# Kernel optimization log

Hardware: AMD Instinct MI355X
Metric: run time of the kernel (lower is better)

## Reference

```python
import jax, jax.numpy as jnp
import numpy as np

N_EMBD = 1024
N_HEAD = 16
HEAD_SIZE = N_EMBD // N_HEAD  # 64
BLOCK_SIZE = 2048
HIDDEN = 2 * N_EMBD  # SwiGLU hidden
LN_EPS = 1e-5


def layernorm(x, w, b):
    m = jnp.mean(x, axis=-1, keepdims=True)
    v = jnp.mean(jnp.square(x - m), axis=-1, keepdims=True)
    return (x - m) * jax.lax.rsqrt(v + LN_EPS) * w + b


def rotate_half(x):
    # interleaved halves, exactly as the torch code: stack((-x2, x1)).reshape
    x1 = x[..., 0::2]
    x2 = x[..., 1::2]
    return jnp.stack((-x2, x1), axis=-1).reshape(x.shape)


def rope_tables(T, hd):
    inv_freq = 1.0 / (10000.0 ** (jnp.arange(0, hd, 2, dtype=jnp.float32) / hd))
    t = jnp.arange(T, dtype=jnp.float32)
    freqs = t[:, None] * inv_freq[None, :]           # [T, hd/2]
    emb = jnp.concatenate([freqs, freqs], axis=-1)   # [T, hd]
    return jnp.cos(emb), jnp.sin(emb)


def setup_inputs() -> dict:
    key = jax.random.key(0)
    ks = jax.random.split(key, 12)
    s = 0.02
    d = {
        "x": jax.random.normal(ks[0], (2, BLOCK_SIZE, N_EMBD), dtype=jnp.float32),
        "ln1_w": jnp.ones((N_EMBD,), jnp.float32),
        "ln1_b": jnp.zeros((N_EMBD,), jnp.float32),
        "ln2_w": jnp.ones((N_EMBD,), jnp.float32),
        "ln2_b": jnp.zeros((N_EMBD,), jnp.float32),
        # per-head projections, stored (H, C, hd); equivalent to x @ W.T in torch
        "Wq": jax.random.normal(ks[1], (N_HEAD, N_EMBD, HEAD_SIZE), jnp.float32) * s,
        "Wk": jax.random.normal(ks[2], (N_HEAD, N_EMBD, HEAD_SIZE), jnp.float32) * s,
        "Wv": jax.random.normal(ks[3], (N_HEAD, N_EMBD, HEAD_SIZE), jnp.float32) * s,
        "proj_w": jax.random.normal(ks[4], (N_EMBD, N_EMBD), jnp.float32) * s,
        "proj_b": jnp.zeros((N_EMBD,), jnp.float32),
        # SwiGLU MLP
        "w_w": jax.random.normal(ks[5], (N_EMBD, HIDDEN), jnp.float32) * s,
        "w_b": jnp.zeros((HIDDEN,), jnp.float32),
        "v_w": jax.random.normal(ks[6], (N_EMBD, HIDDEN), jnp.float32) * s,
        "v_b": jnp.zeros((HIDDEN,), jnp.float32),
        "p_w": jax.random.normal(ks[7], (HIDDEN, N_EMBD), jnp.float32) * s,
        "p_b": jnp.zeros((N_EMBD,), jnp.float32),
    }
    return d


def reference(x, ln1_w, ln1_b, ln2_w, ln2_b, Wq, Wk, Wv, proj_w, proj_b,
              w_w, w_b, v_w, v_b, p_w, p_b):
    B, T, C = x.shape
    # --- attention sub-block ---
    h = layernorm(x, ln1_w, ln1_b)
    q = jnp.einsum('btc,hcd->bhtd', h, Wq)
    k = jnp.einsum('btc,hcd->bhtd', h, Wk)
    v = jnp.einsum('btc,hcd->bhtd', h, Wv)
    cos, sin = rope_tables(T, HEAD_SIZE)  # [T, hd]
    cos = cos[None, None]
    sin = sin[None, None]
    q = q * cos + rotate_half(q) * sin
    k = k * cos + rotate_half(k) * sin
    scale = 1.0 / jnp.sqrt(jnp.float32(HEAD_SIZE))
    scores = jnp.einsum('bhtd,bhsd->bhts', q, k) * scale  # [B,H,T,T]
    causal = jnp.tril(jnp.ones((T, T), dtype=bool))
    scores = jnp.where(causal[None, None], scores, -jnp.inf)
    att = jax.nn.softmax(scores, axis=-1)
    o = jnp.einsum('bhts,bhsd->bhtd', att, v)
    o = o.transpose(0, 2, 1, 3).reshape(B, T, C)  # concat heads
    sa = o @ proj_w + proj_b
    x = x + sa
    # --- SwiGLU FFN sub-block ---
    h2 = layernorm(x, ln2_w, ln2_b)
    a = h2 @ w_w + w_b
    a = a * jax.nn.sigmoid(a)  # swish
    b = h2 @ v_w + v_b
    ff = (a * b) @ p_w + p_b
    return x + ff
```

## Files before the change

kernel.cpp:

```cpp
#include <hip/hip_runtime.h>
#include <math.h>

#define N_EMBD    1024
#define N_HEAD    16
#define HEAD_SIZE 64
#define T_SEQ     2048
#define BATCH     2
#define HIDDEN    2048
#define ROWS      4096

typedef __attribute__((ext_vector_type(8))) short bf16x8;
typedef __attribute__((ext_vector_type(4))) float f32x4;
typedef __attribute__((ext_vector_type(16))) float f32x16;
typedef unsigned short u16;

__device__ __forceinline__ u16 f2bf(float x) {
    union { float f; unsigned u; } v; v.f = x;
    unsigned r = v.u + 0x7fffu + ((v.u >> 16) & 1u);
    return (u16)(r >> 16);
}
__device__ __forceinline__ float bf2f(u16 h) {
    union { unsigned u; float f; } v; v.u = ((unsigned)h) << 16;
    return v.f;
}
__device__ __forceinline__ unsigned cvtpk_bf16(float lo, float hi) {
    unsigned r;
    asm volatile("v_cvt_pk_bf16_f32 %0, %1, %2" : "=v"(r) : "v"(lo), "v"(hi));
    return r;
}
__device__ __forceinline__ void gload16(const void* g, void* lds) {
    __builtin_amdgcn_global_load_lds((const __attribute__((address_space(1))) void*)g,
                                     (__attribute__((address_space(3))) void*)lds, 16, 0, 0);
}

__device__ __forceinline__ void wtrans_body(const float* s, u16* d, int ldS, int ldD,
                                            int k0, int n0, float Ts[64][65])
{
    const int tid = threadIdx.x;
    const int rr = tid >> 4, c4 = (tid & 15) * 4;
#pragma unroll
    for (int i = 0; i < 4; i++) {
        float4 v = *(const float4*)(s + (size_t)(k0 + rr + i * 16) * ldS + n0 + c4);
        Ts[rr + i * 16][c4 + 0] = v.x;
        Ts[rr + i * 16][c4 + 1] = v.y;
        Ts[rr + i * 16][c4 + 2] = v.z;
        Ts[rr + i * 16][c4 + 3] = v.w;
    }
    __syncthreads();
    const int nr = tid >> 2, kc = (tid & 3) * 16;
#pragma unroll
    for (int j = 0; j < 4; j++) {
        u16 t0 = f2bf(Ts[kc + j * 4 + 0][nr]);
        u16 t1 = f2bf(Ts[kc + j * 4 + 1][nr]);
        u16 t2 = f2bf(Ts[kc + j * 4 + 2][nr]);
        u16 t3 = f2bf(Ts[kc + j * 4 + 3][nr]);
        *(ushort4*)(d + (size_t)(n0 + nr) * ldD + k0 + kc + j * 4) = make_ushort4(t0, t1, t2, t3);
    }
}

__global__ __launch_bounds__(256) void wtrans(const float* __restrict__ src, u16* __restrict__ dst,
                                              int ldS, int ldD)
{
    __shared__ float Ts[64][65];
    wtrans_body(src, dst, ldS, ldD, blockIdx.x * 64, blockIdx.y * 64, Ts);
}

__global__ __launch_bounds__(256) void wtrans_qkv(const float* __restrict__ Wq, const float* __restrict__ Wk,
                                                  const float* __restrict__ Wv, u16* __restrict__ dst)
{
    __shared__ float Ts[64][65];
    const int z = blockIdx.z;
    const int which = z >> 4;
    const float* s = (which == 0 ? Wq : (which == 1 ? Wk : Wv)) + (size_t)(z & 15) * 65536;
    wtrans_body(s, dst + (size_t)z * 65536, HEAD_SIZE, N_EMBD, blockIdx.x * 64, 0, Ts);
}

__global__ __launch_bounds__(256) void wtrans_wv(const float* __restrict__ ww, const float* __restrict__ vv,
                                                 u16* __restrict__ dw, u16* __restrict__ dv)
{
    __shared__ float Ts[64][65];
    const int z = blockIdx.z;
    const float* s = (z >> 5) ? vv : ww;
    u16* d = (z >> 5) ? dv : dw;
    wtrans_body(s, d, HIDDEN, N_EMBD, blockIdx.x * 64, (z & 31) * 64, Ts);
}

__global__ __launch_bounds__(256) void ln_kernel(const float* __restrict__ x,
                                                 const float* __restrict__ w,
                                                 const float* __restrict__ b,
                                                 u16* __restrict__ out)
{
    const int row = blockIdx.x;
    const int tid = threadIdx.x;
    const float* xr = x + (size_t)row * N_EMBD;
    float4 v = *(const float4*)(xr + tid * 4);
    float s  = v.x + v.y + v.z + v.w;
    float s2 = v.x*v.x + v.y*v.y + v.z*v.z + v.w*v.w;
#pragma unroll
    for (int off = 32; off; off >>= 1) {
        s  += __shfl_xor(s, off);
        s2 += __shfl_xor(s2, off);
    }
    __shared__ float ss[4], ss2[4];
    if ((tid & 63) == 0) { ss[tid >> 6] = s; ss2[tid >> 6] = s2; }
    __syncthreads();
    s  = ss[0] + ss[1] + ss[2] + ss[3];
    s2 = ss2[0] + ss2[1] + ss2[2] + ss2[3];
    const float mean = s * (1.0f / N_EMBD);
    const float var  = s2 * (1.0f / N_EMBD) - mean * mean;
    const float rstd = rsqrtf(var + 1e-5f);
    float4 wv = *(const float4*)(w + tid * 4);
    float4 bv = *(const float4*)(b + tid * 4);
    ushort4 st = make_ushort4(f2bf((v.x - mean) * rstd * wv.x + bv.x),
                              f2bf((v.y - mean) * rstd * wv.y + bv.y),
                              f2bf((v.z - mean) * rstd * wv.z + bv.z),
                              f2bf((v.w - mean) * rstd * wv.w + bv.w));
    *(ushort4*)(out + (size_t)row * N_EMBD + tid * 4) = st;
}

__global__ __launch_bounds__(256) void rope_kernel(u16* __restrict__ q, u16* __restrict__ k)
{
    const int u = blockIdx.x * 256 + threadIdx.x;
    const int i  = u & 31;
    const int t  = (u >> 5) & (T_SEQ - 1);
    const int bh = u >> 16;
    const size_t base = ((size_t)bh * T_SEQ + t) * HEAD_SIZE + 2 * i;
    const float L = 0.28782313662425572f;
    const int i0 = (2 * i) & 31, i1 = (2 * i + 1) & 31;
    float c0, s0, c1, s1;
    sincosf((float)t * __expf(-(float)i0 * L), &s0, &c0);
    sincosf((float)t * __expf(-(float)i1 * L), &s1, &c1);
    float a0 = bf2f(q[base]), a1 = bf2f(q[base + 1]);
    q[base]     = f2bf(a0 * c0 - a1 * s0);
    q[base + 1] = f2bf(a1 * c1 + a0 * s1);
    float b0 = bf2f(k[base]), b1 = bf2f(k[base + 1]);
    k[base]     = f2bf(b0 * c0 - b1 * s0);
    k[base + 1] = f2bf(b1 * c1 + b0 * s1);
}


__global__ __launch_bounds__(256) void gemm_br(const u16* __restrict__ A, const u16* __restrict__ Bt,
                                               const float* __restrict__ bias, const float* __restrict__ resid,
                                               float* __restrict__ Cf,
                                               int N, int K)
{
    __shared__ __align__(16) u16 As[2][128 * 64];
    __shared__ __align__(16) u16 Bs[2][64 * 64];
    const int tid = threadIdx.x, w = tid >> 6, l = tid & 63, l15 = l & 15, l4 = l >> 4;
    const int wm = w >> 1, wn = w & 1;
    const int n0 = blockIdx.x * 64, m0 = blockIdx.y * 128;
    f32x4 acc[4][2] = {};
    const int NT = K >> 6;

    auto stage = [&](int buf, int k0) {
#pragma unroll
        for (int c = 0; c < 4; c++) {
            const int slot = c * 256 + tid;
            const int row = slot >> 3;
            const int sw = ((slot & 7) * 16) ^ ((row & 7) << 4);
            gload16((const char*)(A + (size_t)(m0 + row) * K + k0) + sw, (char*)&As[buf][0] + slot * 16);
        }
#pragma unroll
        for (int c = 0; c < 2; c++) {
            const int slot = c * 256 + tid;
            const int row = slot >> 3;
            const int sw = ((slot & 7) * 16) ^ ((row & 7) << 4);
            gload16((const char*)(Bt + (size_t)(n0 + row) * K + k0) + sw, (char*)&Bs[buf][0] + slot * 16);
        }
    };

    stage(0, 0);
    __syncthreads();
    int cur = 0;
    for (int t = 0; t < NT; t++) {
        if (t + 1 < NT) stage(cur ^ 1, (t + 1) << 6);
#pragma unroll
        for (int ks = 0; ks < 2; ks++) {
            const int cb = ks * 64 + l4 * 16;
            bf16x8 af[4], bf[2];
#pragma unroll
            for (int mt = 0; mt < 4; mt++) {
                const int row = wm * 64 + mt * 16 + l15;
                af[mt] = *(const bf16x8*)((const char*)&As[cur][0] + row * 128 + (cb ^ ((row & 7) << 4)));
            }
#pragma unroll
            for (int u = 0; u < 2; u++) {
                const int row = wn * 32 + u * 16 + l15;
                bf[u] = *(const bf16x8*)((const char*)&Bs[cur][0] + row * 128 + (cb ^ ((row & 7) << 4)));
            }
#pragma unroll
            for (int mt = 0; mt < 4; mt++)
#pragma unroll
                for (int u = 0; u < 2; u++)
                    acc[mt][u] = __builtin_amdgcn_mfma_f32_16x16x32_bf16(af[mt], bf[u], acc[mt][u], 0, 0, 0);
        }
        __syncthreads();
        cur ^= 1;
    }
#pragma unroll
    for (int mt = 0; mt < 4; mt++) {
#pragma unroll
        for (int u = 0; u < 2; u++) {
            const int n = n0 + wn * 32 + u * 16 + l15;
            const float bi = bias[n];
#pragma unroll
            for (int r = 0; r < 4; r++) {
                const int m = m0 + wm * 64 + mt * 16 + l4 * 4 + r;
                const size_t idx = (size_t)m * N + n;
                Cf[idx] = acc[mt][u][r] + bi + resid[idx];
            }
        }
    }
}

__global__ __launch_bounds__(256, 4) void gemm_qkv(const u16* __restrict__ A, const u16* __restrict__ Bt,
                                                   u16* __restrict__ qo, u16* __restrict__ ko, u16* __restrict__ vto)
{
    __shared__ __align__(16) u16 As[2][64 * 64];
    __shared__ __align__(16) u16 Bs[2][64 * 64];
    const int tid = threadIdx.x, w = tid >> 6, l = tid & 63, l15 = l & 15, l4 = l >> 4;
    const int wm = w >> 1, wn = w & 1;
    const int n0 = blockIdx.x * 128, m0 = blockIdx.y * 128;
    const int K = N_EMBD;
    f32x4 acc[4][4] = {};
    const int NT = K >> 5;

    auto stage = [&](int buf, int k0) {
#pragma unroll
        for (int c = 0; c < 2; c++) {
            const int slot = c * 256 + tid;
            const int r2 = slot >> 3;
            const int w16u = (slot & 7) ^ (r2 & 7);
            const int grow = (w16u >> 2) * 64 + r2;
            const int kc = w16u & 3;
            gload16(A  + (size_t)(m0 + grow) * K + k0 + kc * 8, (char*)&As[buf][0] + slot * 16);
            gload16(Bt + (size_t)(n0 + grow) * K + k0 + kc * 8, (char*)&Bs[buf][0] + slot * 16);
        }
    };

    stage(0, 0);
    __syncthreads();
    int cur = 0;
    for (int t = 0; t < NT; t++) {
        if (t + 1 < NT) stage(cur ^ 1, (t + 1) << 5);
        bf16x8 af[4], bf[4];
#pragma unroll
        for (int q4 = 0; q4 < 4; q4++) {
            const int ga = wm * 64 + q4 * 16 + l15;
            const int ra = ga & 63, ha = ga >> 6;
            af[q4] = *(const bf16x8*)((const char*)&As[cur][0] + ra * 128 + (((ha << 2) | l4) ^ (ra & 7)) * 16);
            const int gb = wn * 64 + q4 * 16 + l15;
            const int rb = gb & 63, hb = gb >> 6;
            bf[q4] = *(const bf16x8*)((const char*)&Bs[cur][0] + rb * 128 + (((hb << 2) | l4) ^ (rb & 7)) * 16);
        }
#pragma unroll
        for (int mt = 0; mt < 4; mt++)
#pragma unroll
            for (int nt = 0; nt < 4; nt++)
                acc[mt][nt] = __builtin_amdgcn_mfma_f32_16x16x32_bf16(af[mt], bf[nt], acc[mt][nt], 0, 0, 0);
        __syncthreads();
        cur ^= 1;
    }
#pragma unroll
    for (int mt = 0; mt < 4; mt++) {
#pragma unroll
        for (int nt = 0; nt < 4; nt++) {
            const int n = n0 + wn * 64 + nt * 16 + l15;
            const int which = n >> 10, hd = (n >> 6) & 15, dd = n & 63;
            const int mb = m0 + wm * 64 + mt * 16 + l4 * 4;
            const int bI = mb >> 11, tq = mb & (T_SEQ - 1);
            if (which == 2) {
                ushort4 st = make_ushort4(f2bf(acc[mt][nt][0]), f2bf(acc[mt][nt][1]),
                                          f2bf(acc[mt][nt][2]), f2bf(acc[mt][nt][3]));
                *(ushort4*)(vto + ((size_t)(bI * N_HEAD + hd) * HEAD_SIZE + dd) * T_SEQ + tq) = st;
            } else {
                u16* dst = (which == 0) ? qo : ko;
#pragma unroll
                for (int r = 0; r < 4; r++)
                    dst[((size_t)(bI * N_HEAD + hd) * T_SEQ + tq + r) * HEAD_SIZE + dd] = f2bf(acc[mt][nt][r]);
            }
        }
    }
}

__global__ __launch_bounds__(256, 4) void gemm_glu(const u16* __restrict__ A, const u16* __restrict__ Bw,
                                                   const u16* __restrict__ Bv,
                                                   const float* __restrict__ wb, const float* __restrict__ vb,
                                                   u16* __restrict__ G)
{
    __shared__ __align__(16) u16 As[2][64 * 64];
    __shared__ __align__(16) u16 Bws[2][32 * 64];
    __shared__ __align__(16) u16 Bvs[2][32 * 64];
    const int tid = threadIdx.x, w = tid >> 6, l = tid & 63, l15 = l & 15, l4 = l >> 4;
    const int wm = w >> 1, wn = w & 1;
    const int n0 = blockIdx.x * 64, m0 = blockIdx.y * 128;
    const int K = N_EMBD;
    f32x4 accA[4][2] = {};
    f32x4 accB[4][2] = {};
    const int NT = K >> 5;

    auto stage = [&](int buf, int k0) {
#pragma unroll
        for (int c = 0; c < 2; c++) {
            const int slot = c * 256 + tid;
            const int r2 = slot >> 3;
            const int w16u = (slot & 7) ^ (r2 & 7);
            const int grow = (w16u >> 2) * 64 + r2;
            const int kc = w16u & 3;
            gload16(A + (size_t)(m0 + grow) * K + k0 + kc * 8, (char*)&As[buf][0] + slot * 16);
        }
        {
            const int slot = tid;
            const int r2 = slot >> 3;
            const int w16u = (slot & 7) ^ (r2 & 7);
            const int grow = (w16u >> 2) * 32 + r2;
            const int kc = w16u & 3;
            gload16(Bw + (size_t)(n0 + grow) * K + k0 + kc * 8, (char*)&Bws[buf][0] + slot * 16);
            gload16(Bv + (size_t)(n0 + grow) * K + k0 + kc * 8, (char*)&Bvs[buf][0] + slot * 16);
        }
    };

    stage(0, 0);
    __syncthreads();
    int cur = 0;
    for (int t = 0; t < NT; t++) {
        if (t + 1 < NT) stage(cur ^ 1, (t + 1) << 5);
        bf16x8 af[4], bwf[2], bvf[2];
#pragma unroll
        for (int q4 = 0; q4 < 4; q4++) {
            const int ga = wm * 64 + q4 * 16 + l15;
            const int ra = ga & 63, ha = ga >> 6;
            af[q4] = *(const bf16x8*)((const char*)&As[cur][0] + ra * 128 + (((ha << 2) | l4) ^ (ra & 7)) * 16);
        }
#pragma unroll
        for (int u = 0; u < 2; u++) {
            const int gb = wn * 32 + u * 16 + l15;
            const int rb = gb & 31, hb = gb >> 5;
            const int off = rb * 128 + (((hb << 2) | l4) ^ (rb & 7)) * 16;
            bwf[u] = *(const bf16x8*)((const char*)&Bws[cur][0] + off);
            bvf[u] = *(const bf16x8*)((const char*)&Bvs[cur][0] + off);
        }
#pragma unroll
        for (int mt = 0; mt < 4; mt++)
#pragma unroll
            for (int u = 0; u < 2; u++) {
                accA[mt][u] = __builtin_amdgcn_mfma_f32_16x16x32_bf16(af[mt], bwf[u], accA[mt][u], 0, 0, 0);
                accB[mt][u] = __builtin_amdgcn_mfma_f32_16x16x32_bf16(af[mt], bvf[u], accB[mt][u], 0, 0, 0);
            }
        __syncthreads();
        cur ^= 1;
    }
#pragma unroll
    for (int mt = 0; mt < 4; mt++) {
#pragma unroll
        for (int u = 0; u < 2; u++) {
            const int n = n0 + wn * 32 + u * 16 + l15;
            const float wbi = wb[n], vbi = vb[n];
#pragma unroll
            for (int r = 0; r < 4; r++) {
                const int m = m0 + wm * 64 + mt * 16 + l4 * 4 + r;
                const float a  = accA[mt][u][r] + wbi;
                const float bb = accB[mt][u][r] + vbi;
                G[(size_t)m * HIDDEN + n] = f2bf(a / (1.f + __expf(-a)) * bb);
            }
        }
    }
}

__global__ __launch_bounds__(256, 2) void attn_mfma(const u16* __restrict__ q, const u16* __restrict__ k,
                                                    const u16* __restrict__ vt, u16* __restrict__ o)
{
    __shared__ __align__(16) u16 Kb[2][128 * 64];
    __shared__ __align__(16) u16 Vb[2][64 * 128];
    __shared__ float ml[2][32];
    const int tid = threadIdx.x, l = tid & 63, l31 = l & 31, hh2 = (l >> 5) & 1;
    const int wid  = tid >> 6;
    const int qsub = wid >> 1;
    const int par  = wid & 1;
    const int bh  = blockIdx.x;
    const int qtb = (int)gridDim.y - 1 - (int)blockIdx.y;
    const int qt  = qtb * 2 + qsub;
    const int qw0 = qt * 32;
    const int nc  = qtb + 1;
    const int npairs = (nc + 1) >> 1;
    const u16* qb  = q  + (size_t)bh * T_SEQ * HEAD_SIZE;
    const u16* kbg = k  + (size_t)bh * T_SEQ * HEAD_SIZE;
    const u16* vbg = vt + (size_t)bh * HEAD_SIZE * T_SEQ;

    bf16x8 qf[4];
    {
        const u16* qr = qb + (size_t)(qw0 + l31) * HEAD_SIZE + hh2 * 8;
#pragma unroll
        for (int kk = 0; kk < 4; kk++) qf[kk] = *(const bf16x8*)(qr + kk * 16);
    }

    f32x16 oacc0 = {}, oacc1 = {};
    float lrow = 0.f;
    const float qs = 0.125f * 1.44269504088896f;
    const float M0 = 20.f;

    auto stage = [&](int buf, int s0p) {
#pragma unroll
        for (int c = 0; c < 4; c++) {
            const int slot = c * 256 + tid;
            const int row = slot >> 3, colb = (slot & 7) * 16;
            const int sw = colb ^ ((row & 7) << 4);
            gload16((const char*)(kbg + (size_t)(s0p + row) * HEAD_SIZE) + sw, (char*)&Kb[buf][0] + slot * 16);
        }
#pragma unroll
        for (int c = 0; c < 4; c++) {
            const int slot = c * 256 + tid;
            const int row = slot >> 4, col16 = slot & 15;
            const int sw = (col16 ^ (row & 15)) << 4;
            gload16((const char*)(vbg + (size_t)row * T_SEQ + s0p) + sw, (char*)&Vb[buf][0] + slot * 16);
        }
    };

    stage(0, 0);
    __syncthreads();
    int cur = 0;

    for (int j = 0; j < npairs; j++) {
        if (j + 1 < npairs) stage(cur ^ 1, (j + 1) * 128);

        const int cc = 2 * j + par;
        if (cc < nc) {
            const bool diag = (cc == nc - 1);
            const bool half = diag && !(qt & 1);

            f32x16 sa0 = {}, sa1 = {};
#pragma unroll
            for (int kk = 0; kk < 4; kk++) {
                const int row = par * 64 + l31;
                const int swz = (row & 7) << 4;
                const bf16x8 kf = *(const bf16x8*)((const char*)&Kb[cur][0] + row * 128 + ((kk * 32 + hh2 * 16) ^ swz));
                sa0 = __builtin_amdgcn_mfma_f32_32x32x16_bf16(kf, qf[kk], sa0, 0, 0, 0);
            }
            if (!half) {
#pragma unroll
                for (int kk = 0; kk < 4; kk++) {
                    const int row = par * 64 + 32 + l31;
                    const int swz = (row & 7) << 4;
                    const bf16x8 kf = *(const bf16x8*)((const char*)&Kb[cur][0] + row * 128 + ((kk * 32 + hh2 * 16) ^ swz));
                    sa1 = __builtin_amdgcn_mfma_f32_32x32x16_bf16(kf, qf[kk], sa1, 0, 0, 0);
                }
            }

            if (diag) {
#pragma unroll
                for (int reg = 0; reg < 16; reg++) {
                    const int R = (reg & 3) + 8 * (reg >> 2) + 4 * hh2;
                    if (R > l31) { if (qt & 1) sa1[reg] = -1e30f; else sa0[reg] = -1e30f; }
                }
            }

            float ls = 0.f;
#pragma unroll
            for (int reg = 0; reg < 16; reg++) {
                const float pv = exp2f(fmaf(sa0[reg], qs, -M0));
                sa0[reg] = pv;
                ls += pv;
            }
            if (!half) {
#pragma unroll
                for (int reg = 0; reg < 16; reg++) {
                    const float pv = exp2f(fmaf(sa1[reg], qs, -M0));
                    sa1[reg] = pv;
                    ls += pv;
                }
            }
            ls += __shfl_xor(ls, 32);
            lrow += ls;

            unsigned pkA[8], pkB[8];
#pragma unroll
            for (int jj = 0; jj < 8; jj++) pkA[jj] = cvtpk_bf16(sa0[2 * jj], sa0[2 * jj + 1]);
            if (!half) {
#pragma unroll
                for (int jj = 0; jj < 8; jj++) pkB[jj] = cvtpk_bf16(sa1[2 * jj], sa1[2 * jj + 1]);
            }

#pragma unroll
            for (int st = 0; st < 4; st++) {
                if (half && st >= 2) continue;
                const unsigned* pk = (st < 2) ? pkA : pkB;
                const int b = (st & 1) * 4;
                union { unsigned u[4]; bf16x8 v; } r;
                const unsigned s0w = (unsigned)__shfl_xor((int)pk[b + 0], 32);
                const unsigned s1w = (unsigned)__shfl_xor((int)pk[b + 1], 32);
                const unsigned s2w = (unsigned)__shfl_xor((int)pk[b + 2], 32);
                const unsigned s3w = (unsigned)__shfl_xor((int)pk[b + 3], 32);
                r.u[0] = hh2 ? s2w : pk[b + 0];
                r.u[1] = hh2 ? s3w : pk[b + 1];
                r.u[2] = hh2 ? pk[b + 2] : s0w;
                r.u[3] = hh2 ? pk[b + 3] : s1w;
#pragma unroll
                for (int dt = 0; dt < 2; dt++) {
                    const int row = dt * 32 + l31;
                    const int col16 = (par * 8 + st * 2 + hh2) ^ (row & 15);
                    const bf16x8 vf = *(const bf16x8*)((const char*)&Vb[cur][0] + row * 256 + col16 * 16);
                    if (dt == 0) oacc0 = __builtin_amdgcn_mfma_f32_32x32x16_bf16(vf, r.v, oacc0, 0, 0, 0);
                    else         oacc1 = __builtin_amdgcn_mfma_f32_32x32x16_bf16(vf, r.v, oacc1, 0, 0, 0);
                }
            }
        }
        __syncthreads();
        cur ^= 1;
    }

    float* obuf = (float*)&Kb[0][0] + (size_t)qsub * 2048;
    if (par == 1) {
#pragma unroll
        for (int reg = 0; reg < 16; reg++) {
            const int R = (reg & 3) + 8 * (reg >> 2) + 4 * hh2;
            obuf[R * 32 + l31] = oacc0[reg];
            obuf[(32 + R) * 32 + l31] = oacc1[reg];
        }
        if (hh2 == 0) ml[qsub][l31] = lrow;
    }
    __syncthreads();
    if (par == 0) {
        const float inv = 1.f / (lrow + ml[qsub][l31]);
        const int bI = bh >> 4, hd = bh & 15;
        u16* ob = o + ((size_t)(bI * T_SEQ + qw0 + l31)) * N_EMBD + hd * HEAD_SIZE;
#pragma unroll
        for (int g = 0; g < 4; g++) {
            const int d0a = g * 8 + hh2 * 4;
            float v0[4], v1[4];
#pragma unroll
            for (int r = 0; r < 4; r++) {
                const int R = d0a + r;
                v0[r] = (oacc0[4 * g + r] + obuf[R * 32 + l31]) * inv;
                v1[r] = (oacc1[4 * g + r] + obuf[(32 + R) * 32 + l31]) * inv;
            }
            *(ushort4*)(ob + d0a)      = make_ushort4(f2bf(v0[0]), f2bf(v0[1]), f2bf(v0[2]), f2bf(v0[3]));
            *(ushort4*)(ob + 32 + d0a) = make_ushort4(f2bf(v1[0]), f2bf(v1[1]), f2bf(v1[2]), f2bf(v1[3]));
        }
    }
}

extern "C" void kernel_launch(void* const* d_in, const int* in_sizes, int n_in,
                              void* d_out, int out_size, void* d_ws, size_t ws_size,
                              hipStream_t stream)
{
    (void)in_sizes; (void)n_in; (void)out_size; (void)ws_size;
    const float* x      = (const float*)d_in[0];
    const float* ln1_w  = (const float*)d_in[1];
    const float* ln1_b  = (const float*)d_in[2];
    const float* ln2_w  = (const float*)d_in[3];
    const float* ln2_b  = (const float*)d_in[4];
    const float* Wq     = (const float*)d_in[5];
    const float* Wk     = (const float*)d_in[6];
    const float* Wv     = (const float*)d_in[7];
    const float* proj_w = (const float*)d_in[8];
    const float* proj_b = (const float*)d_in[9];
    const float* w_w    = (const float*)d_in[10];
    const float* w_b    = (const float*)d_in[11];
    const float* v_w    = (const float*)d_in[12];
    const float* v_b    = (const float*)d_in[13];
    const float* p_w    = (const float*)d_in[14];
    const float* p_b    = (const float*)d_in[15];
    float* out = (float*)d_out;

    char* W = (char*)d_ws;
    u16*   Wqkv = (u16*)(W + 0);
    u16*   pwT  = (u16*)(W + 6291456);
    u16*   wwT  = (u16*)(W + 8388608);
    u16*   vvT  = (u16*)(W + 12582912);
    u16*   ppT  = (u16*)(W + 16777216);
    u16*   h    = (u16*)(W + 20971520);
    u16*   qB   = (u16*)(W + 29360128);
    u16*   kB   = (u16*)(W + 37748736);
    u16*   vtB  = (u16*)(W + 46137344);
    u16*   oB   = (u16*)(W + 54525952);
    float* x1   = (float*)(W + 62914560);
    u16*   ga   = qB;

    wtrans_qkv<<<dim3(16, 1, 48), 256, 0, stream>>>(Wq, Wk, Wv, Wqkv);
    wtrans_wv<<<dim3(16, 1, 64), 256, 0, stream>>>(w_w, v_w, wwT, vvT);
    wtrans<<<dim3(16, 16), 256, 0, stream>>>(proj_w, pwT, 1024, 1024);
    wtrans<<<dim3(32, 16), 256, 0, stream>>>(p_w, ppT, 1024, 2048);

    ln_kernel<<<ROWS, 256, 0, stream>>>(x, ln1_w, ln1_b, h);
    gemm_qkv<<<dim3(24, 32), 256, 0, stream>>>(h, Wqkv, qB, kB, vtB);
    rope_kernel<<<(BATCH * N_HEAD * T_SEQ * 32) / 256, 256, 0, stream>>>(qB, kB);
    attn_mfma<<<dim3(BATCH * N_HEAD, T_SEQ / 64), 256, 0, stream>>>(qB, kB, vtB, oB);
    gemm_br<<<dim3(16, 32), 256, 0, stream>>>(oB, pwT, proj_b, x, x1, N_EMBD, N_EMBD);
    ln_kernel<<<ROWS, 256, 0, stream>>>(x1, ln2_w, ln2_b, h);
    gemm_glu<<<dim3(32, 32), 256, 0, stream>>>(h, wwT, vvT, w_b, v_b, ga);
    gemm_br<<<dim3(16, 32), 256, 0, stream>>>(ga, ppT, p_b, x1, out, N_EMBD, HIDDEN);
}
```

Baseline: 212.7 us.

## Fuse RoPE into QKV GEMM epilogue and shrink attention KV tiles

Removes the standalone RoPE kernel and applies the rotation in the QKV GEMM epilogue, using a lane shuffle to fetch the paired element, so q/k are no longer re-read and re-written. Separately, the attention kernel now stages 64-key tiles instead of 128-key pairs, which halves its shared memory and raises the occupancy hint to 4 blocks, with each wave handling one 32-key half per iteration. The trade-offs are extra sincos work in the GEMM epilogue and more loop iterations and barriers in attention.

```diff
diff --git a/kernel.cpp b/kernel.cpp
--- a/kernel.cpp
+++ b/kernel.cpp
@@ -118,27 +118,6 @@
     *(ushort4*)(out + (size_t)row * N_EMBD + tid * 4) = st;
 }
 
-__global__ __launch_bounds__(256) void rope_kernel(u16* __restrict__ q, u16* __restrict__ k)
-{
-    const int u = blockIdx.x * 256 + threadIdx.x;
-    const int i  = u & 31;
-    const int t  = (u >> 5) & (T_SEQ - 1);
-    const int bh = u >> 16;
-    const size_t base = ((size_t)bh * T_SEQ + t) * HEAD_SIZE + 2 * i;
-    const float L = 0.28782313662425572f;
-    const int i0 = (2 * i) & 31, i1 = (2 * i + 1) & 31;
-    float c0, s0, c1, s1;
-    sincosf((float)t * __expf(-(float)i0 * L), &s0, &c0);
-    sincosf((float)t * __expf(-(float)i1 * L), &s1, &c1);
-    float a0 = bf2f(q[base]), a1 = bf2f(q[base + 1]);
-    q[base]     = f2bf(a0 * c0 - a1 * s0);
-    q[base + 1] = f2bf(a1 * c1 + a0 * s1);
-    float b0 = bf2f(k[base]), b1 = bf2f(k[base + 1]);
-    k[base]     = f2bf(b0 * c0 - b1 * s0);
-    k[base + 1] = f2bf(b1 * c1 + b0 * s1);
-}
-
-
 __global__ __launch_bounds__(256) void gemm_br(const u16* __restrict__ A, const u16* __restrict__ Bt,
                                                const float* __restrict__ bias, const float* __restrict__ resid,
                                                float* __restrict__ Cf,
@@ -261,6 +240,7 @@
         __syncthreads();
         cur ^= 1;
     }
+    const float Lr = 0.28782313662425572f;
 #pragma unroll
     for (int mt = 0; mt < 4; mt++) {
 #pragma unroll
@@ -275,9 +255,16 @@
                 *(ushort4*)(vto + ((size_t)(bI * N_HEAD + hd) * HEAD_SIZE + dd) * T_SEQ + tq) = st;
             } else {
                 u16* dst = (which == 0) ? qo : ko;
-#pragma unroll
-                for (int r = 0; r < 4; r++)
-                    dst[((size_t)(bI * N_HEAD + hd) * T_SEQ + tq + r) * HEAD_SIZE + dd] = f2bf(acc[mt][nt][r]);
+                const float fr = __expf(-(float)(dd & 31) * Lr);
+#pragma unroll
+                for (int r = 0; r < 4; r++) {
+                    const float v = acc[mt][nt][r];
+                    const float part = __shfl_xor(v, 1);
+                    float sn, cs;
+                    sincosf((float)(tq + r) * fr, &sn, &cs);
+                    const float ov = (dd & 1) ? fmaf(v, cs, part * sn) : fmaf(v, cs, -part * sn);
+                    dst[((size_t)(bI * N_HEAD + hd) * T_SEQ + tq + r) * HEAD_SIZE + dd] = f2bf(ov);
+                }
             }
         }
     }
@@ -367,11 +354,11 @@
     }
 }
 
-__global__ __launch_bounds__(256, 2) void attn_mfma(const u16* __restrict__ q, const u16* __restrict__ k,
+__global__ __launch_bounds__(256, 4) void attn_mfma(const u16* __restrict__ q, const u16* __restrict__ k,
                                                     const u16* __restrict__ vt, u16* __restrict__ o)
 {
-    __shared__ __align__(16) u16 Kb[2][128 * 64];
-    __shared__ __align__(16) u16 Vb[2][64 * 128];
+    __shared__ __align__(16) u16 Kb[2][64 * 64];
+    __shared__ __align__(16) u16 Vb[2][64 * 64];
     __shared__ float ml[2][32];
     const int tid = threadIdx.x, l = tid & 63, l31 = l & 31, hh2 = (l >> 5) & 1;
     const int wid  = tid >> 6;
@@ -382,7 +369,6 @@
     const int qt  = qtb * 2 + qsub;
     const int qw0 = qt * 32;
     const int nc  = qtb + 1;
-    const int npairs = (nc + 1) >> 1;
     const u16* qb  = q  + (size_t)bh * T_SEQ * HEAD_SIZE;
     const u16* kbg = k  + (size_t)bh * T_SEQ * HEAD_SIZE;
     const u16* vbg = vt + (size_t)bh * HEAD_SIZE * T_SEQ;
@@ -399,20 +385,20 @@
     const float qs = 0.125f * 1.44269504088896f;
     const float M0 = 20.f;
 
-    auto stage = [&](int buf, int s0p) {
-#pragma unroll
-        for (int c = 0; c < 4; c++) {
+    auto stage = [&](int buf, int s0) {
+#pragma unroll
+        for (int c = 0; c < 2; c++) {
             const int slot = c * 256 + tid;
-            const int row = slot >> 3, colb = (slot & 7) * 16;
-            const int sw = colb ^ ((row & 7) << 4);
-            gload16((const char*)(kbg + (size_t)(s0p + row) * HEAD_SIZE) + sw, (char*)&Kb[buf][0] + slot * 16);
-        }
-#pragma unroll
-        for (int c = 0; c < 4; c++) {
+            const int row = slot >> 3;
+            const int sw = ((slot & 7) * 16) ^ ((row & 7) << 4);
+            gload16((const char*)(kbg + (size_t)(s0 + row) * HEAD_SIZE) + sw, (char*)&Kb[buf][0] + slot * 16);
+        }
+#pragma unroll
+        for (int c = 0; c < 2; c++) {
             const int slot = c * 256 + tid;
-            const int row = slot >> 4, col16 = slot & 15;
-            const int sw = (col16 ^ (row & 15)) << 4;
-            gload16((const char*)(vbg + (size_t)row * T_SEQ + s0p) + sw, (char*)&Vb[buf][0] + slot * 16);
+            const int row = slot >> 3;
+            const int sw = ((slot & 7) * 16) ^ ((row & 7) << 4);
+            gload16((const char*)(vbg + (size_t)row * T_SEQ + s0) + sw, (char*)&Vb[buf][0] + slot * 16);
         }
     };
 
@@ -420,71 +406,43 @@
     __syncthreads();
     int cur = 0;
 
-    for (int j = 0; j < npairs; j++) {
-        if (j + 1 < npairs) stage(cur ^ 1, (j + 1) * 128);
-
-        const int cc = 2 * j + par;
-        if (cc < nc) {
-            const bool diag = (cc == nc - 1);
-            const bool half = diag && !(qt & 1);
-
-            f32x16 sa0 = {}, sa1 = {};
+    for (int j = 0; j < nc; j++) {
+        if (j + 1 < nc) stage(cur ^ 1, (j + 1) * 64);
+
+        const int hc = 2 * j + par;
+        if (hc <= qt) {
+            f32x16 sa = {};
+            const int row = par * 32 + l31;
+            const int swz = (row & 7) << 4;
 #pragma unroll
             for (int kk = 0; kk < 4; kk++) {
-                const int row = par * 64 + l31;
-                const int swz = (row & 7) << 4;
                 const bf16x8 kf = *(const bf16x8*)((const char*)&Kb[cur][0] + row * 128 + ((kk * 32 + hh2 * 16) ^ swz));
-                sa0 = __builtin_amdgcn_mfma_f32_32x32x16_bf16(kf, qf[kk], sa0, 0, 0, 0);
-            }
-            if (!half) {
-#pragma unroll
-                for (int kk = 0; kk < 4; kk++) {
-                    const int row = par * 64 + 32 + l31;
-                    const int swz = (row & 7) << 4;
-                    const bf16x8 kf = *(const bf16x8*)((const char*)&Kb[cur][0] + row * 128 + ((kk * 32 + hh2 * 16) ^ swz));
-                    sa1 = __builtin_amdgcn_mfma_f32_32x32x16_bf16(kf, qf[kk], sa1, 0, 0, 0);
-                }
-            }
-
-            if (diag) {
+                sa = __builtin_amdgcn_mfma_f32_32x32x16_bf16(kf, qf[kk], sa, 0, 0, 0);
+            }
+            if (hc == qt) {
 #pragma unroll
                 for (int reg = 0; reg < 16; reg++) {
                     const int R = (reg & 3) + 8 * (reg >> 2) + 4 * hh2;
-                    if (R > l31) { if (qt & 1) sa1[reg] = -1e30f; else sa0[reg] = -1e30f; }
+                    if (R > l31) sa[reg] = -1e30f;
                 }
             }
-
             float ls = 0.f;
 #pragma unroll
             for (int reg = 0; reg < 16; reg++) {
-                const float pv = exp2f(fmaf(sa0[reg], qs, -M0));
-                sa0[reg] = pv;
+                const float pv = exp2f(fmaf(sa[reg], qs, -M0));
+                sa[reg] = pv;
                 ls += pv;
-            }
-            if (!half) {
-#pragma unroll
-                for (int reg = 0; reg < 16; reg++) {
-                    const float pv = exp2f(fmaf(sa1[reg], qs, -M0));
-                    sa1[reg] = pv;
-                    ls += pv;
-                }
             }
             ls += __shfl_xor(ls, 32);
             lrow += ls;
 
-            unsigned pkA[8], pkB[8];
-#pragma unroll
-            for (int jj = 0; jj < 8; jj++) pkA[jj] = cvtpk_bf16(sa0[2 * jj], sa0[2 * jj + 1]);
-            if (!half) {
-#pragma unroll
-                for (int jj = 0; jj < 8; jj++) pkB[jj] = cvtpk_bf16(sa1[2 * jj], sa1[2 * jj + 1]);
-            }
-
-#pragma unroll
-            for (int st = 0; st < 4; st++) {
-                if (half && st >= 2) continue;
-                const unsigned* pk = (st < 2) ? pkA : pkB;
-                const int b = (st & 1) * 4;
+            unsigned pk[8];
+#pragma unroll
+            for (int jj = 0; jj < 8; jj++) pk[jj] = cvtpk_bf16(sa[2 * jj], sa[2 * jj + 1]);
+
+#pragma unroll
+            for (int st = 0; st < 2; st++) {
+                const int b = st * 4;
                 union { unsigned u[4]; bf16x8 v; } r;
                 const unsigned s0w = (unsigned)__shfl_xor((int)pk[b + 0], 32);
                 const unsigned s1w = (unsigned)__shfl_xor((int)pk[b + 1], 32);
@@ -496,9 +454,10 @@
                 r.u[3] = hh2 ? pk[b + 3] : s1w;
 #pragma unroll
                 for (int dt = 0; dt < 2; dt++) {
-                    const int row = dt * 32 + l31;
-                    const int col16 = (par * 8 + st * 2 + hh2) ^ (row & 15);
-                    const bf16x8 vf = *(const bf16x8*)((const char*)&Vb[cur][0] + row * 256 + col16 * 16);
+                    const int vrow = dt * 32 + l31;
+                    const int vswz = (vrow & 7) << 4;
+                    const int vcol = (par * 64 + st * 32 + hh2 * 16) ^ vswz;
+                    const bf16x8 vf = *(const bf16x8*)((const char*)&Vb[cur][0] + vrow * 128 + vcol);
                     if (dt == 0) oacc0 = __builtin_amdgcn_mfma_f32_32x32x16_bf16(vf, r.v, oacc0, 0, 0, 0);
                     else         oacc1 = __builtin_amdgcn_mfma_f32_32x32x16_bf16(vf, r.v, oacc1, 0, 0, 0);
                 }
@@ -583,7 +542,6 @@
 
     ln_kernel<<<ROWS, 256, 0, stream>>>(x, ln1_w, ln1_b, h);
     gemm_qkv<<<dim3(24, 32), 256, 0, stream>>>(h, Wqkv, qB, kB, vtB);
-    rope_kernel<<<(BATCH * N_HEAD * T_SEQ * 32) / 256, 256, 0, stream>>>(qB, kB);
     attn_mfma<<<dim3(BATCH * N_HEAD, T_SEQ / 64), 256, 0, stream>>>(qB, kB, vtB, oB);
     gemm_br<<<dim3(16, 32), 256, 0, stream>>>(oB, pwT, proj_b, x, x1, N_EMBD, N_EMBD);
     ln_kernel<<<ROWS, 256, 0, stream>>>(x1, ln2_w, ln2_b, h);
```

Result: slower. 652.0 us (+206.5%).
